# Optimization experiments

Hardware: AMD Instinct MI355X
Metric: run time of the kernel (lower is better)

## Reference

```python
import jax, jax.numpy as jnp
import numpy as np


def _xavier(key, shape):
    fan_out, fan_in = shape[0], shape[1]
    lim = np.sqrt(6.0 / (fan_in + fan_out)).astype(np.float32)
    return jax.random.uniform(key, shape, jnp.float32, -lim, lim)


def setup_inputs() -> dict:
    key = jax.random.key(0)
    ks = jax.random.split(key, 28)
    B, D, G, ND = 16384, 32, 6, 8
    V_user, V_item, V_gender, V_age, V_occ, V_genre = 1000000, 100000, 2, 7, 21, 19
    H1, H2 = 128, 64
    deep_in = 6 * D + ND  # 200
    return {
        "user_id": jax.random.randint(ks[0], (B,), 0, V_user),
        "item_id": jax.random.randint(ks[1], (B,), 0, V_item),
        "user_gender": jax.random.randint(ks[2], (B,), 0, V_gender),
        "user_age": jax.random.randint(ks[3], (B,), 0, V_age),
        "user_occupation": jax.random.randint(ks[4], (B,), 0, V_occ),
        "item_genre_ids": jax.random.randint(ks[5], (B, G), 0, V_genre),
        "item_genre_mask": jax.random.randint(ks[6], (B, G), 0, 2).astype(jnp.float32),
        "dense_features": jax.random.normal(ks[7], (B, ND), jnp.float32),
        # first-order (1-dim) embedding tables
        "fo_user": _xavier(ks[8], (V_user, 1)),
        "fo_item": _xavier(ks[9], (V_item, 1)),
        "fo_gender": _xavier(ks[10], (V_gender, 1)),
        "fo_age": _xavier(ks[11], (V_age, 1)),
        "fo_occ": _xavier(ks[12], (V_occ, 1)),
        "fo_genre": _xavier(ks[13], (V_genre, 1)),
        # second-order / deep embedding tables
        "emb_user": _xavier(ks[14], (V_user, D)),
        "emb_item": _xavier(ks[15], (V_item, D)),
        "emb_gender": _xavier(ks[16], (V_gender, D)),
        "emb_age": _xavier(ks[17], (V_age, D)),
        "emb_occ": _xavier(ks[18], (V_occ, D)),
        "emb_genre": _xavier(ks[19], (V_genre, D)),
        # dense linear + deep MLP
        "dense_W": _xavier(ks[20], (1, ND)),
        "dense_b": jnp.zeros((1,), jnp.float32),
        "W1": _xavier(ks[21], (H1, deep_in)),
        "b1": jnp.zeros((H1,), jnp.float32),
        "W2": _xavier(ks[22], (H2, H1)),
        "b2": jnp.zeros((H2,), jnp.float32),
        "Wout": _xavier(ks[23], (1, H2)),
        "bout": jnp.zeros((1,), jnp.float32),
    }


def _pool(table, ids, mask):
    # masked mean-pool over the genre list axis
    e = table[ids]                       # [B, G, d]
    m = mask[..., None]                  # [B, G, 1]
    denom = jnp.clip(m.sum(axis=1), 1.0)  # [B, 1]
    return (e * m).sum(axis=1) / denom   # [B, d]


def reference(user_id, item_id, user_gender, user_age, user_occupation,
              item_genre_ids, item_genre_mask, dense_features,
              fo_user, fo_item, fo_gender, fo_age, fo_occ, fo_genre,
              emb_user, emb_item, emb_gender, emb_age, emb_occ, emb_genre,
              dense_W, dense_b, W1, b1, W2, b2, Wout, bout):
    # FM first order: sum of 1-dim gathers + pooled genre + dense linear -> [B,1]
    first = (fo_user[user_id] + fo_item[item_id] + fo_gender[user_gender]
             + fo_age[user_age] + fo_occ[user_occupation]
             + _pool(fo_genre, item_genre_ids, item_genre_mask)
             + dense_features @ dense_W.T + dense_b)
    # FM second order: stack field embeddings [B, 6, D]
    x = jnp.stack([emb_user[user_id], emb_item[item_id], emb_gender[user_gender],
                   emb_age[user_age], emb_occ[user_occupation],
                   _pool(emb_genre, item_genre_ids, item_genre_mask)], axis=1)
    s = x.sum(axis=1)                                   # [B, D]
    second = 0.5 * (s * s - (x * x).sum(axis=1)).sum(axis=1, keepdims=True)  # [B,1]
    # deep part (dropout is identity in eval mode)
    deep_in = jnp.concatenate([x.reshape(x.shape[0], -1), dense_features], axis=1)
    h = jax.nn.relu(deep_in @ W1.T + b1)
    h = jax.nn.relu(h @ W2.T + b2)
    deep = h @ Wout.T + bout                            # [B,1]
    return (first + second + deep).squeeze(1)           # [B]
```

## Files before the change

kernel.cpp:

```cpp
#include <hip/hip_runtime.h>


typedef float v2f __attribute__((ext_vector_type(2)));
static __device__ __forceinline__ v2f bc2(float x) { v2f r; r.x = x; r.y = x; return r; }

#define ROWS_PER_BLOCK 32
#define ROWS_PER_WAVE 8
#define DI_STRIDE 204
#define H1_STRIDE 132

__global__ void pack_weights(const float* __restrict__ W1, const float* __restrict__ W2,
                             float4* __restrict__ W1p, float4* __restrict__ W2p) {
    const int idx = blockIdx.x * blockDim.x + threadIdx.x;
    if (idx < 6400) {
        const int s = idx & 1, jp = (idx >> 1) & 15, k4 = (idx >> 5) % 50, w = idx / 1600;
        const int j0 = w * 32 + 2 * jp, c = 4 * k4 + 2 * s;
        W1p[idx] = make_float4(W1[j0 * 200 + c],     W1[(j0 + 1) * 200 + c],
                               W1[j0 * 200 + c + 1], W1[(j0 + 1) * 200 + c + 1]);
    }
    if (idx < 2048) {
        const int s = idx & 1, jp = (idx >> 1) & 7, k4 = (idx >> 4) & 31, w = idx >> 9;
        const int j0 = w * 16 + 2 * jp, c = 4 * k4 + 2 * s;
        W2p[idx] = make_float4(W2[j0 * 128 + c],     W2[(j0 + 1) * 128 + c],
                               W2[j0 * 128 + c + 1], W2[(j0 + 1) * 128 + c + 1]);
    }
}

__global__ __launch_bounds__(256) void deepfm_kernel(
    const int* __restrict__ user_id, const int* __restrict__ item_id,
    const int* __restrict__ gender_, const int* __restrict__ age_,
    const int* __restrict__ occ_, const int* __restrict__ genre_ids,
    const float* __restrict__ genre_mask, const float* __restrict__ dense,
    const float* __restrict__ fo_user, const float* __restrict__ fo_item,
    const float* __restrict__ fo_gender, const float* __restrict__ fo_age,
    const float* __restrict__ fo_occ, const float* __restrict__ fo_genre,
    const float* __restrict__ emb_user, const float* __restrict__ emb_item,
    const float* __restrict__ emb_gender, const float* __restrict__ emb_age,
    const float* __restrict__ emb_occ, const float* __restrict__ emb_genre,
    const float* __restrict__ dense_W, const float* __restrict__ dense_b,
    const float4* __restrict__ W1p, const float* __restrict__ b1,
    const float4* __restrict__ W2p, const float* __restrict__ b2,
    const float* __restrict__ Wout, const float* __restrict__ bout,
    float* __restrict__ out, int B)
{
    __shared__ float lds_di[ROWS_PER_BLOCK][DI_STRIDE];
    __shared__ float lds_rs[ROWS_PER_BLOCK];
    __shared__ float lds_part[ROWS_PER_BLOCK][4];

    const int tid = threadIdx.x;
    const int wid = tid >> 6;
    const int lane = tid & 63;
    const int blockRow0 = blockIdx.x * ROWS_PER_BLOCK;

    {
        const int rowBase = blockRow0 + wid * ROWS_PER_WAVE;
        int uid[ROWS_PER_WAVE], iid[ROWS_PER_WAVE], gg[ROWS_PER_WAVE],
            aa[ROWS_PER_WAVE], oo[ROWS_PER_WAVE];
        #pragma unroll
        for (int r = 0; r < ROWS_PER_WAVE; ++r) {
            int row = rowBase + r; if (row >= B) row = B - 1;
            uid[r] = user_id[row]; iid[r] = item_id[row];
            gg[r] = gender_[row];  aa[r] = age_[row];  oo[r] = occ_[row];
        }

        #pragma unroll
        for (int r = 0; r < ROWS_PER_WAVE; ++r) {
            int row = rowBase + r; if (row >= B) row = B - 1;
            const int ri = wid * ROWS_PER_WAVE + r;

            int gid[6]; float mk[6]; float msum = 0.f;
            #pragma unroll
            for (int t = 0; t < 6; ++t) {
                gid[t] = genre_ids[row * 6 + t];
                mk[t]  = genre_mask[row * 6 + t];
                msum  += mk[t];
            }
            const float inv_den = 1.0f / fmaxf(msum, 1.0f);

            float pe_sum = 0.f, pe_sq = 0.f;
            {
                float v = (lane < 32) ? emb_user[(size_t)uid[r] * 32 + lane]
                                      : emb_item[(size_t)iid[r] * 32 + (lane - 32)];
                lds_di[ri][lane] = v;
                pe_sum += v; pe_sq += v * v;
            }
            {
                float v = (lane < 32) ? emb_gender[gg[r] * 32 + lane]
                                      : emb_age[aa[r] * 32 + (lane - 32)];
                lds_di[ri][64 + lane] = v;
                pe_sum += v; pe_sq += v * v;
            }
            {
                float v;
                if (lane < 32) {
                    v = emb_occ[oo[r] * 32 + lane];
                } else {
                    const int d = lane - 32;
                    float s = 0.f;
                    #pragma unroll
                    for (int t = 0; t < 6; ++t) s += mk[t] * emb_genre[gid[t] * 32 + d];
                    v = s * inv_den;
                }
                lds_di[ri][128 + lane] = v;
                pe_sum += v; pe_sq += v * v;
            }
            if (lane < 8) lds_di[ri][192 + lane] = dense[(size_t)row * 8 + lane];

            float s2 = pe_sum + __shfl_xor(pe_sum, 32);
            float ss = pe_sq  + __shfl_xor(pe_sq, 32);
            float t2 = 0.5f * (s2 * s2 - ss);
            #pragma unroll
            for (int off = 16; off >= 1; off >>= 1) t2 += __shfl_xor(t2, off);

            float fo = fo_user[uid[r]] + fo_item[iid[r]] + fo_gender[gg[r]]
                     + fo_age[aa[r]] + fo_occ[oo[r]];
            float fg = 0.f;
            #pragma unroll
            for (int t = 0; t < 6; ++t) fg += mk[t] * fo_genre[gid[t]];
            fo += fg * inv_den;
            float dd = 0.f;
            #pragma unroll
            for (int j = 0; j < 8; ++j) dd += dense[(size_t)row * 8 + j] * dense_W[j];
            fo += dd + dense_b[0];

            if (lane == 0) lds_rs[ri] = fo + t2;
        }
    }
    __syncthreads();

    const int jp1 = lane & 15;
    const int rh  = lane >> 4;

    v2f acc[ROWS_PER_WAVE];
    #pragma unroll
    for (int r = 0; r < ROWS_PER_WAVE; ++r) acc[r] = bc2(0.f);

    {
        const float4* __restrict__ W1b = W1p + wid * 1600;
        const float4* __restrict__ dv = reinterpret_cast<const float4*>(&lds_di[0][0]);

        for (int k4 = 0; k4 < 50; ++k4) {
            const float4 wa = W1b[(k4 * 16 + jp1) * 2 + 0];
            const float4 wb = W1b[(k4 * 16 + jp1) * 2 + 1];
            const v2f w0 = { wa.x, wa.y }, w1 = { wa.z, wa.w };
            const v2f w2 = { wb.x, wb.y }, w3 = { wb.z, wb.w };
            #pragma unroll
            for (int r = 0; r < ROWS_PER_WAVE; ++r) {
                const float4 a = dv[(rh + 4 * r) * 51 + k4];
                acc[r] = __builtin_elementwise_fma(w0, bc2(a.x), acc[r]);
                acc[r] = __builtin_elementwise_fma(w1, bc2(a.y), acc[r]);
                acc[r] = __builtin_elementwise_fma(w2, bc2(a.z), acc[r]);
                acc[r] = __builtin_elementwise_fma(w3, bc2(a.w), acc[r]);
            }
        }
    }
    __syncthreads();

    float* __restrict__ h1b = &lds_di[0][0];
    {
        const int j0 = wid * 32 + 2 * jp1;
        const float2 bb = *reinterpret_cast<const float2*>(b1 + j0);
        #pragma unroll
        for (int r = 0; r < ROWS_PER_WAVE; ++r) {
            const int row = rh + 4 * r;
            reinterpret_cast<float2*>(h1b)[(row * H1_STRIDE + j0) >> 1] =
                make_float2(fmaxf(acc[r].x + bb.x, 0.f), fmaxf(acc[r].y + bb.y, 0.f));
        }
    }
    __syncthreads();

    const int jp2 = lane & 7;
    const int rh2 = lane >> 3;

    v2f acc2[4];
    #pragma unroll
    for (int t = 0; t < 4; ++t) acc2[t] = bc2(0.f);

    {
        const float4* __restrict__ W2b = W2p + wid * 512;
        const float4* __restrict__ h1v = reinterpret_cast<const float4*>(h1b);

        for (int k4 = 0; k4 < 32; ++k4) {
            const float4 wa = W2b[(k4 * 8 + jp2) * 2 + 0];
            const float4 wb = W2b[(k4 * 8 + jp2) * 2 + 1];
            const v2f w0 = { wa.x, wa.y }, w1 = { wa.z, wa.w };
            const v2f w2 = { wb.x, wb.y }, w3 = { wb.z, wb.w };
            #pragma unroll
            for (int t = 0; t < 4; ++t) {
                const float4 h = h1v[(rh2 + 8 * t) * 33 + k4];
                acc2[t] = __builtin_elementwise_fma(w0, bc2(h.x), acc2[t]);
                acc2[t] = __builtin_elementwise_fma(w1, bc2(h.y), acc2[t]);
                acc2[t] = __builtin_elementwise_fma(w2, bc2(h.z), acc2[t]);
                acc2[t] = __builtin_elementwise_fma(w3, bc2(h.w), acc2[t]);
            }
        }
    }

    {
        const int j0 = wid * 16 + 2 * jp2;
        const float2 bb2 = *reinterpret_cast<const float2*>(b2 + j0);
        const float2 wo  = *reinterpret_cast<const float2*>(Wout + j0);
        #pragma unroll
        for (int t = 0; t < 4; ++t) {
            const float h2x = fmaxf(acc2[t].x + bb2.x, 0.f);
            const float h2y = fmaxf(acc2[t].y + bb2.y, 0.f);
            float v = wo.x * h2x + wo.y * h2y;
            v += __shfl_xor(v, 1); v += __shfl_xor(v, 2); v += __shfl_xor(v, 4);
            if (jp2 == 0) lds_part[rh2 + 8 * t][wid] = v;
        }
    }
    __syncthreads();

    if (tid < ROWS_PER_BLOCK) {
        const int row = blockRow0 + tid;
        if (row < B) {
            const float deep = lds_part[tid][0] + lds_part[tid][1]
                             + lds_part[tid][2] + lds_part[tid][3] + bout[0];
            out[row] = deep + lds_rs[tid];
        }
    }
}

extern "C" void kernel_launch(void* const* d_in, const int* in_sizes, int n_in,
                              void* d_out, int out_size, void* d_ws, size_t ws_size,
                              hipStream_t stream) {
    const int B = in_sizes[0];

    float4* W1p = reinterpret_cast<float4*>(d_ws);
    float4* W2p = reinterpret_cast<float4*>((char*)d_ws + 102400);

    pack_weights<<<25, 256, 0, stream>>>(
        (const float*)d_in[22], (const float*)d_in[24], W1p, W2p);

    const int grid = (B + ROWS_PER_BLOCK - 1) / ROWS_PER_BLOCK;
    deepfm_kernel<<<grid, 256, 0, stream>>>(
        (const int*)d_in[0],  (const int*)d_in[1],  (const int*)d_in[2],
        (const int*)d_in[3],  (const int*)d_in[4],  (const int*)d_in[5],
        (const float*)d_in[6],  (const float*)d_in[7],
        (const float*)d_in[8],  (const float*)d_in[9],  (const float*)d_in[10],
        (const float*)d_in[11], (const float*)d_in[12], (const float*)d_in[13],
        (const float*)d_in[14], (const float*)d_in[15], (const float*)d_in[16],
        (const float*)d_in[17], (const float*)d_in[18], (const float*)d_in[19],
        (const float*)d_in[20], (const float*)d_in[21],
        W1p, (const float*)d_in[23],
        W2p, (const float*)d_in[25],
        (const float*)d_in[26], (const float*)d_in[27],
        (float*)d_out, B);
}
```

Before: 258.6 us.

## Remap MLP register tiling to 8 outputs by 2 rows per lane

Changes the per-lane tile of both MLP layers. Each lane now computes 8 (then 4) output neurons for 2 rows, where before it computed 2 neurons for 8 (then 4) rows, and the packed weight layouts are rewritten to match. The intent is fewer LDS activation reads per FMA, at the cost of more global/L2 weight loads per lane and lower reuse of each weight across rows. The shuffle reduction at the output shrinks to two steps.

```diff
diff --git a/kernel.cpp b/kernel.cpp
--- a/kernel.cpp
+++ b/kernel.cpp
@@ -3,6 +3,7 @@
 
 typedef float v2f __attribute__((ext_vector_type(2)));
 static __device__ __forceinline__ v2f bc2(float x) { v2f r; r.x = x; r.y = x; return r; }
+static __device__ __forceinline__ float relu1(float x) { return fmaxf(x, 0.f); }
 
 #define ROWS_PER_BLOCK 32
 #define ROWS_PER_WAVE 8
@@ -13,16 +14,18 @@
                              float4* __restrict__ W1p, float4* __restrict__ W2p) {
     const int idx = blockIdx.x * blockDim.x + threadIdx.x;
     if (idx < 6400) {
-        const int s = idx & 1, jp = (idx >> 1) & 15, k4 = (idx >> 5) % 50, w = idx / 1600;
-        const int j0 = w * 32 + 2 * jp, c = 4 * k4 + 2 * s;
-        W1p[idx] = make_float4(W1[j0 * 200 + c],     W1[(j0 + 1) * 200 + c],
-                               W1[j0 * 200 + c + 1], W1[(j0 + 1) * 200 + c + 1]);
+        const int q = idx & 7, rest = idx >> 3;
+        const int k4 = rest % 50, o = rest / 50;
+        const int j = o * 8 + 2 * (q >> 1), c = 4 * k4 + 2 * (q & 1);
+        W1p[idx] = make_float4(W1[j * 200 + c],     W1[(j + 1) * 200 + c],
+                               W1[j * 200 + c + 1], W1[(j + 1) * 200 + c + 1]);
     }
     if (idx < 2048) {
-        const int s = idx & 1, jp = (idx >> 1) & 7, k4 = (idx >> 4) & 31, w = idx >> 9;
-        const int j0 = w * 16 + 2 * jp, c = 4 * k4 + 2 * s;
-        W2p[idx] = make_float4(W2[j0 * 128 + c],     W2[(j0 + 1) * 128 + c],
-                               W2[j0 * 128 + c + 1], W2[(j0 + 1) * 128 + c + 1]);
+        const int q = idx & 3, rest = idx >> 2;
+        const int k4 = rest & 31, o = rest >> 5;
+        const int j = o * 4 + 2 * (q >> 1), c = 4 * k4 + 2 * (q & 1);
+        W2p[idx] = make_float4(W2[j * 128 + c],     W2[(j + 1) * 128 + c],
+                               W2[j * 128 + c + 1], W2[(j + 1) * 128 + c + 1]);
     }
 }
 
@@ -128,29 +131,39 @@
     }
     __syncthreads();
 
-    const int jp1 = lane & 15;
-    const int rh  = lane >> 4;
-
-    v2f acc[ROWS_PER_WAVE];
+    const int jpg = lane & 3;
+    const int rh  = lane >> 2;
+
+    v2f acc[2][4];
     #pragma unroll
-    for (int r = 0; r < ROWS_PER_WAVE; ++r) acc[r] = bc2(0.f);
-
-    {
-        const float4* __restrict__ W1b = W1p + wid * 1600;
+    for (int r = 0; r < 2; ++r)
+        #pragma unroll
+        for (int p = 0; p < 4; ++p) acc[r][p] = bc2(0.f);
+
+    {
+        const float4* __restrict__ W1b = W1p + (wid * 4 + jpg) * 400;
         const float4* __restrict__ dv = reinterpret_cast<const float4*>(&lds_di[0][0]);
 
         for (int k4 = 0; k4 < 50; ++k4) {
-            const float4 wa = W1b[(k4 * 16 + jp1) * 2 + 0];
-            const float4 wb = W1b[(k4 * 16 + jp1) * 2 + 1];
-            const v2f w0 = { wa.x, wa.y }, w1 = { wa.z, wa.w };
-            const v2f w2 = { wb.x, wb.y }, w3 = { wb.z, wb.w };
-            #pragma unroll
-            for (int r = 0; r < ROWS_PER_WAVE; ++r) {
-                const float4 a = dv[(rh + 4 * r) * 51 + k4];
-                acc[r] = __builtin_elementwise_fma(w0, bc2(a.x), acc[r]);
-                acc[r] = __builtin_elementwise_fma(w1, bc2(a.y), acc[r]);
-                acc[r] = __builtin_elementwise_fma(w2, bc2(a.z), acc[r]);
-                acc[r] = __builtin_elementwise_fma(w3, bc2(a.w), acc[r]);
+            float4 wq[8];
+            #pragma unroll
+            for (int q = 0; q < 8; ++q) wq[q] = W1b[k4 * 8 + q];
+            const float4 a0 = dv[rh * 51 + k4];
+            const float4 a1 = dv[(rh + 16) * 51 + k4];
+            #pragma unroll
+            for (int p = 0; p < 4; ++p) {
+                const v2f w0 = { wq[2 * p].x,     wq[2 * p].y };
+                const v2f w1 = { wq[2 * p].z,     wq[2 * p].w };
+                const v2f w2 = { wq[2 * p + 1].x, wq[2 * p + 1].y };
+                const v2f w3 = { wq[2 * p + 1].z, wq[2 * p + 1].w };
+                acc[0][p] = __builtin_elementwise_fma(w0, bc2(a0.x), acc[0][p]);
+                acc[0][p] = __builtin_elementwise_fma(w1, bc2(a0.y), acc[0][p]);
+                acc[0][p] = __builtin_elementwise_fma(w2, bc2(a0.z), acc[0][p]);
+                acc[0][p] = __builtin_elementwise_fma(w3, bc2(a0.w), acc[0][p]);
+                acc[1][p] = __builtin_elementwise_fma(w0, bc2(a1.x), acc[1][p]);
+                acc[1][p] = __builtin_elementwise_fma(w1, bc2(a1.y), acc[1][p]);
+                acc[1][p] = __builtin_elementwise_fma(w2, bc2(a1.z), acc[1][p]);
+                acc[1][p] = __builtin_elementwise_fma(w3, bc2(a1.w), acc[1][p]);
             }
         }
     }
@@ -158,55 +171,69 @@
 
     float* __restrict__ h1b = &lds_di[0][0];
     {
-        const int j0 = wid * 32 + 2 * jp1;
-        const float2 bb = *reinterpret_cast<const float2*>(b1 + j0);
-        #pragma unroll
-        for (int r = 0; r < ROWS_PER_WAVE; ++r) {
-            const int row = rh + 4 * r;
-            reinterpret_cast<float2*>(h1b)[(row * H1_STRIDE + j0) >> 1] =
-                make_float2(fmaxf(acc[r].x + bb.x, 0.f), fmaxf(acc[r].y + bb.y, 0.f));
-        }
-    }
-    __syncthreads();
-
-    const int jp2 = lane & 7;
-    const int rh2 = lane >> 3;
-
-    v2f acc2[4];
+        const int j0 = (wid * 4 + jpg) * 8;
+        const float4 b_lo = *reinterpret_cast<const float4*>(b1 + j0);
+        const float4 b_hi = *reinterpret_cast<const float4*>(b1 + j0 + 4);
+        #pragma unroll
+        for (int r = 0; r < 2; ++r) {
+            const int row = rh + 16 * r;
+            const float4 lo = make_float4(relu1(acc[r][0].x + b_lo.x), relu1(acc[r][0].y + b_lo.y),
+                                          relu1(acc[r][1].x + b_lo.z), relu1(acc[r][1].y + b_lo.w));
+            const float4 hi = make_float4(relu1(acc[r][2].x + b_hi.x), relu1(acc[r][2].y + b_hi.y),
+                                          relu1(acc[r][3].x + b_hi.z), relu1(acc[r][3].y + b_hi.w));
+            reinterpret_cast<float4*>(h1b + row * H1_STRIDE + j0)[0] = lo;
+            reinterpret_cast<float4*>(h1b + row * H1_STRIDE + j0)[1] = hi;
+        }
+    }
+    __syncthreads();
+
+    v2f acc2[2][2];
     #pragma unroll
-    for (int t = 0; t < 4; ++t) acc2[t] = bc2(0.f);
-
-    {
-        const float4* __restrict__ W2b = W2p + wid * 512;
+    for (int r = 0; r < 2; ++r)
+        #pragma unroll
+        for (int p = 0; p < 2; ++p) acc2[r][p] = bc2(0.f);
+
+    {
+        const float4* __restrict__ W2b = W2p + (wid * 4 + jpg) * 128;
         const float4* __restrict__ h1v = reinterpret_cast<const float4*>(h1b);
 
         for (int k4 = 0; k4 < 32; ++k4) {
-            const float4 wa = W2b[(k4 * 8 + jp2) * 2 + 0];
-            const float4 wb = W2b[(k4 * 8 + jp2) * 2 + 1];
-            const v2f w0 = { wa.x, wa.y }, w1 = { wa.z, wa.w };
-            const v2f w2 = { wb.x, wb.y }, w3 = { wb.z, wb.w };
-            #pragma unroll
-            for (int t = 0; t < 4; ++t) {
-                const float4 h = h1v[(rh2 + 8 * t) * 33 + k4];
-                acc2[t] = __builtin_elementwise_fma(w0, bc2(h.x), acc2[t]);
-                acc2[t] = __builtin_elementwise_fma(w1, bc2(h.y), acc2[t]);
-                acc2[t] = __builtin_elementwise_fma(w2, bc2(h.z), acc2[t]);
-                acc2[t] = __builtin_elementwise_fma(w3, bc2(h.w), acc2[t]);
-            }
-        }
-    }
-
-    {
-        const int j0 = wid * 16 + 2 * jp2;
-        const float2 bb2 = *reinterpret_cast<const float2*>(b2 + j0);
-        const float2 wo  = *reinterpret_cast<const float2*>(Wout + j0);
-        #pragma unroll
-        for (int t = 0; t < 4; ++t) {
-            const float h2x = fmaxf(acc2[t].x + bb2.x, 0.f);
-            const float h2y = fmaxf(acc2[t].y + bb2.y, 0.f);
-            float v = wo.x * h2x + wo.y * h2y;
-            v += __shfl_xor(v, 1); v += __shfl_xor(v, 2); v += __shfl_xor(v, 4);
-            if (jp2 == 0) lds_part[rh2 + 8 * t][wid] = v;
+            float4 wq[4];
+            #pragma unroll
+            for (int q = 0; q < 4; ++q) wq[q] = W2b[k4 * 4 + q];
+            const float4 a0 = h1v[rh * 33 + k4];
+            const float4 a1 = h1v[(rh + 16) * 33 + k4];
+            #pragma unroll
+            for (int p = 0; p < 2; ++p) {
+                const v2f w0 = { wq[2 * p].x,     wq[2 * p].y };
+                const v2f w1 = { wq[2 * p].z,     wq[2 * p].w };
+                const v2f w2 = { wq[2 * p + 1].x, wq[2 * p + 1].y };
+                const v2f w3 = { wq[2 * p + 1].z, wq[2 * p + 1].w };
+                acc2[0][p] = __builtin_elementwise_fma(w0, bc2(a0.x), acc2[0][p]);
+                acc2[0][p] = __builtin_elementwise_fma(w1, bc2(a0.y), acc2[0][p]);
+                acc2[0][p] = __builtin_elementwise_fma(w2, bc2(a0.z), acc2[0][p]);
+                acc2[0][p] = __builtin_elementwise_fma(w3, bc2(a0.w), acc2[0][p]);
+                acc2[1][p] = __builtin_elementwise_fma(w0, bc2(a1.x), acc2[1][p]);
+                acc2[1][p] = __builtin_elementwise_fma(w1, bc2(a1.y), acc2[1][p]);
+                acc2[1][p] = __builtin_elementwise_fma(w2, bc2(a1.z), acc2[1][p]);
+                acc2[1][p] = __builtin_elementwise_fma(w3, bc2(a1.w), acc2[1][p]);
+            }
+        }
+    }
+
+    {
+        const int j0 = (wid * 4 + jpg) * 4;
+        const float4 bb2 = *reinterpret_cast<const float4*>(b2 + j0);
+        const float4 wo  = *reinterpret_cast<const float4*>(Wout + j0);
+        #pragma unroll
+        for (int r = 0; r < 2; ++r) {
+            const float h0 = relu1(acc2[r][0].x + bb2.x);
+            const float h1x = relu1(acc2[r][0].y + bb2.y);
+            const float h2x = relu1(acc2[r][1].x + bb2.z);
+            const float h3x = relu1(acc2[r][1].y + bb2.w);
+            float v = wo.x * h0 + wo.y * h1x + wo.z * h2x + wo.w * h3x;
+            v += __shfl_xor(v, 1); v += __shfl_xor(v, 2);
+            if (jpg == 0) lds_part[rh + 16 * r][wid] = v;
         }
     }
     __syncthreads();
```

After: 393.8 us. 1.52x slower.
